# Performance work log

Hardware: AMD Instinct MI355X
Metric: run time of the kernel (lower is better)

Reference implementation:

```python
import jax, jax.numpy as jnp
import numpy as np

TINY = 1e-8
B, T, D = 128, 32, 400


def _offsets(T):
    offs, off = [], 0
    for lvl in range(T):
        offs.append(off)
        off += T - lvl
    return offs


def _inside_indices(T):
    # For level l, span start i (L = T - l spans), split k in [0, l):
    #   left child  = cell(offs[k] + i)             (span (i, level k))
    #   right child = cell(offs[l-k-1] + i + k + 1) (span (i+k+1, level l-k-1))
    offs = _offsets(T)
    out = {}
    for level in range(1, T):
        L = T - level
        lidx = np.empty((L, level), np.int32)
        ridx = np.empty((L, level), np.int32)
        for i in range(L):
            for k in range(level):
                lidx[i, k] = offs[k] + i
                ridx[i, k] = offs[level - k - 1] + i + k + 1
        out[level] = (jnp.asarray(lidx.reshape(-1)), jnp.asarray(ridx.reshape(-1)))
    return offs, out


def unit_norm(x):
    n = jnp.sqrt(jnp.sum(x * x, axis=-1, keepdims=True))
    return x / jnp.maximum(n, TINY)


def setup_inputs() -> dict:
    key = jax.random.key(0)
    ks = jax.random.split(key, 12)
    sc = 1.0 / np.sqrt(D).astype(np.float32)
    return {
        'x': jax.random.normal(ks[0], (B, T, D), jnp.float32),
        'w_leaf_h': jax.random.normal(ks[1], (D, D), jnp.float32) * sc,
        'b_leaf_h': jax.random.normal(ks[2], (D,), jnp.float32) * sc,
        'w_leaf_c': jax.random.normal(ks[3], (D, D), jnp.float32) * sc,
        'b_leaf_c': jax.random.normal(ks[4], (D,), jnp.float32) * sc,
        'u_lh': jax.random.normal(ks[5], (D, D), jnp.float32) * sc,
        'u_rh': jax.random.normal(ks[6], (D, D), jnp.float32) * sc,
        'b_h': jax.random.normal(ks[7], (D,), jnp.float32) * sc,
        'u_lc': jax.random.normal(ks[8], (D, D), jnp.float32) * sc,
        'u_rc': jax.random.normal(ks[9], (D, D), jnp.float32) * sc,
        'b_c': jax.random.normal(ks[10], (D,), jnp.float32) * sc,
        'w_score': jax.random.normal(ks[11], (D, D), jnp.float32) * sc,
    }


def reference(x, w_leaf_h, b_leaf_h, w_leaf_c, b_leaf_c,
              u_lh, u_rh, b_h, u_lc, u_rc, b_c, w_score):
    Bb, Tt, Dd = x.shape
    offs, idx = _inside_indices(Tt)
    ncells = Tt * (Tt + 1) // 2
    # leaf_transform + unit normalize
    h0 = unit_norm(jnp.tanh(x @ w_leaf_h + b_leaf_h))
    c0 = unit_norm(jnp.tanh(x @ w_leaf_c + b_leaf_c))
    ch = jnp.zeros((Bb, ncells, Dd), x.dtype).at[:, :Tt].set(h0)
    cc = jnp.zeros((Bb, ncells, Dd), x.dtype).at[:, :Tt].set(c0)
    cs = jnp.zeros((Bb, ncells, 1), x.dtype)
    for level in range(1, Tt):  # fixed structural loop over tree levels
        L, N = Tt - level, level
        lidx, ridx = idx[level]
        lh, rh = ch[:, lidx], ch[:, ridx]  # gather: [B, L*N, D]
        lc, rc = cc[:, lidx], cc[:, ridx]
        ls, rs = cs[:, lidx], cs[:, ridx]  # [B, L*N, 1]
        # compose
        h = jnp.tanh(lh @ u_lh + rh @ u_rh + b_h)
        c = jnp.tanh(lc @ u_lc + rc @ u_rc + b_c)
        # bilinear score + child scores, softmax over splits N
        s = jnp.einsum('bnd,de,bne->bn', lh, w_score, rh)[..., None] + ls + rs
        s = s.reshape(Bb, L, N, 1)
        p = jax.nn.softmax(s, axis=2)
        h_agg = unit_norm(jnp.sum(h.reshape(Bb, L, N, Dd) * p, axis=2))
        c_agg = unit_norm(jnp.sum(c.reshape(Bb, L, N, Dd) * p, axis=2))
        s_agg = jnp.sum(s * p, axis=2)
        off = offs[level]
        ch = ch.at[:, off:off + L].set(h_agg)
        cc = cc.at[:, off:off + L].set(c_agg)
        cs = cs.at[:, off:off + L].set(s_agg)
    return ch
```

## Files before the change

### kernel.cpp

```cpp
#include <hip/hip_runtime.h>
#include <hip/hip_bf16.h>
#include <stdint.h>


#define BB 128
#define TT 32
#define DD 400
#define NCELLS 528
#define NW 2000
#define KP 416

typedef __hip_bfloat16 bf16_t;
typedef __attribute__((ext_vector_type(8))) short s8v;
typedef __attribute__((ext_vector_type(4))) float f32x4;

__device__ __forceinline__ int offs_of(int v) { return v * TT - (v * (v - 1)) / 2; }

__device__ __forceinline__ float asf(uint32_t bits) {
    union { uint32_t i; float f; } v; v.i = bits; return v.f;
}
__device__ __forceinline__ uint16_t f2bf(float f) {
    union { float f; uint32_t i; } v; v.f = f;
    uint32_t x = v.i;
    return (uint16_t)((x + 0x7fffu + ((x >> 16) & 1u)) >> 16);
}

__device__ __forceinline__ float tanh_fast(float x) {
    float e = __builtin_amdgcn_exp2f(x * 2.8853900817779268f);
    return 1.f - 2.f * __builtin_amdgcn_rcpf(e + 1.f);
}

__device__ __forceinline__ void block_reduce2(float& a, float& b, float* sred) {
#pragma unroll
    for (int o = 32; o > 0; o >>= 1) { a += __shfl_down(a, o); b += __shfl_down(b, o); }
    int lane = threadIdx.x & 63, w = threadIdx.x >> 6;
    if (lane == 0) { sred[w] = a; sred[4 + w] = b; }
    __syncthreads();
    a = sred[0] + sred[1] + sred[2] + sred[3];
    b = sred[4] + sred[5] + sred[6] + sred[7];
    __syncthreads();
}

__global__ void pack_k(const float* __restrict__ u_lh, const float* __restrict__ u_rh,
                       const float* __restrict__ w_score, const float* __restrict__ u_lc,
                       const float* __restrict__ u_rc, const float* __restrict__ w_leaf_h,
                       const float* __restrict__ w_leaf_c, const float* __restrict__ x,
                       uint16_t* __restrict__ WT, uint16_t* __restrict__ WLT,
                       uint16_t* __restrict__ XB) {
    int idx = blockIdx.x * blockDim.x + threadIdx.x;
    const int nWT = NW * KP, nWLT = 800 * KP, nXB = 4096 * KP;
    if (idx < nWT) {
        int n = idx / KP, k = idx - n * KP;
        float v = 0.f;
        if (k < DD) {
            const float* src = (n < 400) ? u_lh : (n < 800) ? u_rh : (n < 1200) ? w_score
                               : (n < 1600) ? u_lc : u_rc;
            v = src[k * DD + (n % 400)];
        }
        WT[idx] = f2bf(v);
    } else if (idx < nWT + nWLT) {
        int q = idx - nWT; int n = q / KP, k = q - n * KP;
        float v = 0.f;
        if (k < DD) v = (n < 400) ? w_leaf_h[k * DD + n] : w_leaf_c[k * DD + (n - 400)];
        WLT[q] = f2bf(v);
    } else if (idx < nWT + nWLT + nXB) {
        int q = idx - nWT - nWLT; int r = q / KP, k = q - r * KP;
        XB[q] = f2bf(k < DD ? x[(size_t)r * DD + k] : 0.f);
    }
}

__global__ __launch_bounds__(256)
void tgemm_k(const uint16_t* __restrict__ HB, const uint16_t* __restrict__ CB,
             const uint16_t* __restrict__ WT,
             uint16_t* __restrict__ LP, uint16_t* __restrict__ RP, uint16_t* __restrict__ G,
             float* __restrict__ PREout, int mode, int Lcur, int cellbase) {
    __shared__ short As[256][40];
    __shared__ short Ws[80][40];
    const int t = threadIdx.x, lane = t & 63, w = t >> 6;
    const int n0 = blockIdx.x * 80;
    const int tile_m = blockIdx.y * 256;
    const bool cside = (mode == 0) && (n0 >= 1200);
    const int Mtot = (mode == 1) ? 4096 : 128 * Lcur;

    const int arow_l = t >> 2, asub = t & 3;
    const uint16_t* aptr[4];
#pragma unroll
    for (int p = 0; p < 4; p++) {
        int gr = tile_m + arow_l + 64 * p;
        if (gr >= Mtot) gr = 0;
        const uint16_t* base;
        if (mode == 1) {
            base = HB + (size_t)gr * KP;
        } else {
            int rb = gr / Lcur, ri = gr - rb * Lcur;
            base = cside ? CB + (size_t)(rb * 32 + ri) * DD
                         : HB + (size_t)(rb * NCELLS + cellbase + ri) * DD;
        }
        aptr[p] = base + asub * 8;
    }
    const uint16_t* wptr0 = WT + (size_t)(n0 + (t >> 2)) * KP + (t & 3) * 8;
    const uint16_t* wptr1 = WT + (size_t)(n0 + 64 + (t >> 2)) * KP + (t & 3) * 8;

    const int frow = lane & 15, kcol = (lane >> 4) * 8;
    f32x4 acc[4][5];
#pragma unroll
    for (int mi = 0; mi < 4; mi++)
#pragma unroll
        for (int ni = 0; ni < 5; ni++) acc[mi][ni] = (f32x4)(0.f);

    for (int k0 = 0; k0 < KP; k0 += 32) {
        s8v av[4];
#pragma unroll
        for (int p = 0; p < 4; p++) av[p] = *(const s8v*)(aptr[p] + k0);
        s8v wv0 = *(const s8v*)(wptr0 + k0);
        s8v wv1;
        if (t < 64) wv1 = *(const s8v*)(wptr1 + k0);
        __syncthreads();
#pragma unroll
        for (int p = 0; p < 4; p++) *(s8v*)&As[arow_l + 64 * p][asub * 8] = av[p];
        *(s8v*)&Ws[t >> 2][(t & 3) * 8] = wv0;
        if (t < 64) *(s8v*)&Ws[64 + (t >> 2)][(t & 3) * 8] = wv1;
        __syncthreads();
        s8v a[4];
#pragma unroll
        for (int mi = 0; mi < 4; mi++)
            a[mi] = *(const s8v*)&As[64 * w + 16 * mi + frow][kcol];
#pragma unroll
        for (int ni = 0; ni < 5; ni++) {
            s8v bv = *(const s8v*)&Ws[16 * ni + frow][kcol];
#pragma unroll
            for (int mi = 0; mi < 4; mi++)
                acc[mi][ni] = __builtin_amdgcn_mfma_f32_16x16x32_bf16(a[mi], bv, acc[mi][ni], 0, 0, 0);
        }
    }

    const int seg = n0 / 400, ncb = n0 % 400;
    uint16_t* tb = (seg == 2) ? G : (seg == 0 || seg == 3) ? LP : RP;
    const int slot = (seg >= 3) ? 1 : 0;
#pragma unroll
    for (int mi = 0; mi < 4; mi++) {
        int rbase = tile_m + 64 * w + 16 * mi + 4 * (lane >> 4);
#pragma unroll
        for (int i = 0; i < 4; i++) {
            int gr = rbase + i;
            if (gr >= Mtot) continue;
            if (mode == 1) {
                float* o = PREout + (size_t)gr * 800 + n0 + frow;
#pragma unroll
                for (int ni = 0; ni < 5; ni++) o[16 * ni] = acc[mi][ni][i];
            } else {
                int rb = gr / Lcur, ri = gr - rb * Lcur;
                size_t row = (size_t)(rb * NCELLS + cellbase + ri);
                if (seg == 2) {
                    uint16_t* o = tb + row * 400 + ncb + frow;
#pragma unroll
                    for (int ni = 0; ni < 5; ni++) o[16 * ni] = f2bf(acc[mi][ni][i]);
                } else {
                    uint16_t* o = tb + row * 800 + 2 * (ncb + frow) + slot;
#pragma unroll
                    for (int ni = 0; ni < 5; ni++) o[32 * ni] = f2bf(acc[mi][ni][i]);
                }
            }
        }
    }
}

__global__ __launch_bounds__(256)
void leaf_norm_k(const float* __restrict__ PRE, const float* __restrict__ blh,
                 const float* __restrict__ blc, float* __restrict__ Hchart,
                 uint16_t* __restrict__ HB, uint16_t* __restrict__ CB,
                 float* __restrict__ cs) {
    const int r = blockIdx.x;
    const int b = r >> 5, tt = r & 31;
    const int t = threadIdx.x;
    const int d = t * 2;
    float th0 = 0, th1 = 0, tc0 = 0, tc1 = 0;
    if (d < DD) {
        const float* p = PRE + (size_t)r * 800;
        th0 = tanh_fast(p[d] + blh[d]);
        th1 = tanh_fast(p[d + 1] + blh[d + 1]);
        tc0 = tanh_fast(p[400 + d] + blc[d]);
        tc1 = tanh_fast(p[400 + d + 1] + blc[d + 1]);
    }
    __shared__ float sred[8];
    float nh = th0 * th0 + th1 * th1, nc = tc0 * tc0 + tc1 * tc1;
    block_reduce2(nh, nc, sred);
    float rh = 1.f / fmaxf(sqrtf(nh), 1e-8f);
    float rc = 1.f / fmaxf(sqrtf(nc), 1e-8f);
    if (d < DD) {
        size_t ho = (size_t)(b * NCELLS + tt) * DD + d;
        float h0 = th0 * rh, h1 = th1 * rh, c0 = tc0 * rc, c1 = tc1 * rc;
        Hchart[ho] = h0; Hchart[ho + 1] = h1;
        *(uint32_t*)(HB + ho) = (uint32_t)f2bf(h0) | ((uint32_t)f2bf(h1) << 16);
        *(uint32_t*)(CB + (size_t)(b * 32 + tt) * DD + d) =
            (uint32_t)f2bf(c0) | ((uint32_t)f2bf(c1) << 16);
    }
    if (t == 0) cs[b * NCELLS + tt] = 0.f;
}

__global__ __launch_bounds__(256)
void level_k(float* __restrict__ Hchart, uint16_t* __restrict__ HB,
             uint16_t* __restrict__ CB, float* __restrict__ cs,
             const uint16_t* __restrict__ LP, const uint16_t* __restrict__ RP,
             const uint16_t* __restrict__ G,
             const float* __restrict__ b_h, const float* __restrict__ b_c, int level) {
    const int L = TT - level, N = level;
    const int blk = blockIdx.x;
    const int b = blk / L, i = blk - b * L;
    const int cell = offs_of(level) + i;
    const int t = threadIdx.x, lane = t & 63, w = t >> 6;
    __shared__ float sh_s[32], sh_p[32];
    __shared__ float sred[8];

    for (int k = w; k < N; k += 4) {
        int lcell = offs_of(k) + i;
        int rcell = offs_of(level - k - 1) + i + k + 1;
        const uint32_t* g = (const uint32_t*)(G + (size_t)(b * NCELLS + lcell) * DD);
        const uint32_t* hr = (const uint32_t*)(HB + (size_t)(b * NCELLS + rcell) * DD);
        float s = 0.f;
        for (int d2 = lane; d2 < 200; d2 += 64) {
            uint32_t gv = g[d2], hv = hr[d2];
            s += asf(gv << 16) * asf(hv << 16)
               + asf(gv & 0xffff0000u) * asf(hv & 0xffff0000u);
        }
#pragma unroll
        for (int o = 32; o > 0; o >>= 1) s += __shfl_down(s, o);
        if (lane == 0) sh_s[k] = s + cs[b * NCELLS + lcell] + cs[b * NCELLS + rcell];
    }
    __syncthreads();

    if (t == 0) {
        float m = -1e30f;
        for (int k = 0; k < N; k++) m = fmaxf(m, sh_s[k]);
        float sum = 0.f;
        for (int k = 0; k < N; k++) {
            float e = __builtin_amdgcn_exp2f((sh_s[k] - m) * 1.4426950408889634f);
            sh_p[k] = e; sum += e;
        }
        float inv = 1.f / sum, sagg = 0.f;
        for (int k = 0; k < N; k++) { sh_p[k] *= inv; sagg += sh_p[k] * sh_s[k]; }
        cs[b * NCELLS + cell] = sagg;
    }
    __syncthreads();

    float ha0 = 0, ha1 = 0, ca0 = 0, ca1 = 0;
    const int d = t * 2;
    if (d < DD) {
        const float bh0 = b_h[d], bh1 = b_h[d + 1], bc0 = b_c[d], bc1 = b_c[d + 1];
        const uint16_t* lpb = LP + (size_t)(b * NCELLS) * 800 + 2 * d;
        const uint16_t* rpb = RP + (size_t)(b * NCELLS) * 800 + 2 * d;
        for (int k = 0; k < N; k++) {
            float p = sh_p[k];
            int lcell = offs_of(k) + i;
            int rcell = offs_of(level - k - 1) + i + k + 1;
            uint2 lv = *(const uint2*)(lpb + (size_t)lcell * 800);
            uint2 rv = *(const uint2*)(rpb + (size_t)rcell * 800);
            ha0 += p * tanh_fast(asf(lv.x << 16) + asf(rv.x << 16) + bh0);
            ca0 += p * tanh_fast(asf(lv.x & 0xffff0000u) + asf(rv.x & 0xffff0000u) + bc0);
            ha1 += p * tanh_fast(asf(lv.y << 16) + asf(rv.y << 16) + bh1);
            ca1 += p * tanh_fast(asf(lv.y & 0xffff0000u) + asf(rv.y & 0xffff0000u) + bc1);
        }
    }
    float nh = ha0 * ha0 + ha1 * ha1, nc = ca0 * ca0 + ca1 * ca1;
    block_reduce2(nh, nc, sred);
    float rh = 1.f / fmaxf(sqrtf(nh), 1e-8f);
    float rc = 1.f / fmaxf(sqrtf(nc), 1e-8f);
    if (d < DD) {
        float h0 = ha0 * rh, h1 = ha1 * rh, c0 = ca0 * rc, c1 = ca1 * rc;
        size_t ho = (size_t)(b * NCELLS + cell) * DD + d;
        Hchart[ho] = h0; Hchart[ho + 1] = h1;
        *(uint32_t*)(HB + ho) = (uint32_t)f2bf(h0) | ((uint32_t)f2bf(h1) << 16);
        *(uint32_t*)(CB + (size_t)(b * 32 + i) * DD + d) =
            (uint32_t)f2bf(c0) | ((uint32_t)f2bf(c1) << 16);
    }
}

extern "C" void kernel_launch(void* const* d_in, const int* in_sizes, int n_in,
                              void* d_out, int out_size, void* d_ws, size_t ws_size,
                              hipStream_t stream) {
    const float* x        = (const float*)d_in[0];
    const float* w_leaf_h = (const float*)d_in[1];
    const float* b_leaf_h = (const float*)d_in[2];
    const float* w_leaf_c = (const float*)d_in[3];
    const float* b_leaf_c = (const float*)d_in[4];
    const float* u_lh     = (const float*)d_in[5];
    const float* u_rh     = (const float*)d_in[6];
    const float* b_h      = (const float*)d_in[7];
    const float* u_lc     = (const float*)d_in[8];
    const float* u_rc     = (const float*)d_in[9];
    const float* b_c      = (const float*)d_in[10];
    const float* w_score  = (const float*)d_in[11];
    float* Hchart = (float*)d_out;

    const size_t PL = (size_t)BB * NCELLS * DD;
    char* p = (char*)d_ws;
    uint16_t* LP = (uint16_t*)p; p += 2 * PL * sizeof(uint16_t);
    uint16_t* RP = (uint16_t*)p; p += 2 * PL * sizeof(uint16_t);
    uint16_t* G  = (uint16_t*)p; p += PL * sizeof(uint16_t);
    uint16_t* HB = (uint16_t*)p; p += PL * sizeof(uint16_t) + 64;
    uint16_t* CB = (uint16_t*)p; p += (size_t)BB * 32 * DD * sizeof(uint16_t) + 64;
    float* CS    = (float*)p;    p += (size_t)BB * NCELLS * sizeof(float);
    uint16_t* WT = (uint16_t*)p; p += (size_t)NW * KP * sizeof(uint16_t);
    float* PRE    = (float*)LP;
    uint16_t* WLT = RP;
    uint16_t* XB  = RP + (size_t)800 * KP;

    {
        int total = NW * KP + 800 * KP + 4096 * KP;
        pack_k<<<(total + 255) / 256, 256, 0, stream>>>(u_lh, u_rh, w_score, u_lc, u_rc,
                                                        w_leaf_h, w_leaf_c, x, WT, WLT, XB);
    }
    tgemm_k<<<dim3(10, 16), 256, 0, stream>>>(XB, nullptr, WLT, nullptr, nullptr, nullptr,
                                              PRE, 1, 32, 0);
    leaf_norm_k<<<BB * TT, 256, 0, stream>>>(PRE, b_leaf_h, b_leaf_c, Hchart, HB, CB, CS);
    tgemm_k<<<dim3(25, 16), 256, 0, stream>>>(HB, CB, WT, LP, RP, G, nullptr, 0, 32, 0);

    int off = TT;
    for (int level = 1; level < TT; ++level) {
        int L = TT - level;
        level_k<<<BB * L, 256, 0, stream>>>(Hchart, HB, CB, CS, LP, RP, G, b_h, b_c, level);
        if (level < TT - 1) {
            int mby = (128 * L + 255) / 256;
            tgemm_k<<<dim3(25, mby), 256, 0, stream>>>(HB, CB, WT, LP, RP, G, nullptr, 0, L, off);
        }
        off += L;
    }
}
```

Baseline: 1.648 ms.

## Fuse per-level kernels into one persistent cooperative kernel with grid sync

Replaces the roughly 61 per-level kernel launches (level_k plus tgemm_k for each tree level) with a single cooperative persistent kernel. Blocks loop over level cells and GEMM tiles and separate phases with grid.sync(). The GEMM tiles shrink from 256 to 128 rows so the small upper levels have more tiles to spread across the grid. This removes launch overhead and tail gaps between many small kernels, at the cost of grid-wide barriers, capped occupancy (launch bounds 256,2), and a fallback path if the cooperative launch fails.

```diff
diff --git a/kernel.cpp b/kernel.cpp
--- a/kernel.cpp
+++ b/kernel.cpp
@@ -1,6 +1,9 @@
 #include <hip/hip_runtime.h>
+#include <hip/hip_cooperative_groups.h>
 #include <hip/hip_bf16.h>
 #include <stdint.h>
+
+namespace cg = cooperative_groups;
 
 
 #define BB 128
@@ -10,7 +13,6 @@
 #define NW 2000
 #define KP 416
 
-typedef __hip_bfloat16 bf16_t;
 typedef __attribute__((ext_vector_type(8))) short s8v;
 typedef __attribute__((ext_vector_type(4))) float f32x4;
 
@@ -24,7 +26,6 @@
     uint32_t x = v.i;
     return (uint16_t)((x + 0x7fffu + ((x >> 16) & 1u)) >> 16);
 }
-
 __device__ __forceinline__ float tanh_fast(float x) {
     float e = __builtin_amdgcn_exp2f(x * 2.8853900817779268f);
     return 1.f - 2.f * __builtin_amdgcn_rcpf(e + 1.f);
@@ -69,16 +70,14 @@
     }
 }
 
-__global__ __launch_bounds__(256)
-void tgemm_k(const uint16_t* __restrict__ HB, const uint16_t* __restrict__ CB,
-             const uint16_t* __restrict__ WT,
-             uint16_t* __restrict__ LP, uint16_t* __restrict__ RP, uint16_t* __restrict__ G,
-             float* __restrict__ PREout, int mode, int Lcur, int cellbase) {
-    __shared__ short As[256][40];
-    __shared__ short Ws[80][40];
+__device__ __forceinline__
+void tgemm_tile(const uint16_t* __restrict__ HB, const uint16_t* __restrict__ CB,
+                const uint16_t* __restrict__ WT,
+                uint16_t* __restrict__ LP, uint16_t* __restrict__ RP,
+                uint16_t* __restrict__ G, float* __restrict__ PREout,
+                int mode, int Lcur, int cellbase, int n0, int tile_m,
+                short (*As)[40], short (*Ws)[40]) {
     const int t = threadIdx.x, lane = t & 63, w = t >> 6;
-    const int n0 = blockIdx.x * 80;
-    const int tile_m = blockIdx.y * 256;
     const bool cside = (mode == 0) && (n0 >= 1200);
     const int Mtot = (mode == 1) ? 4096 : 128 * Lcur;
 
@@ -160,6 +159,93 @@
 #pragma unroll
                     for (int ni = 0; ni < 5; ni++) o[32 * ni] = f2bf(acc[mi][ni][i]);
                 }
+            }
+        }
+    }
+}
+
+__global__ __launch_bounds__(256)
+void tgemm_k(const uint16_t* __restrict__ HB, const uint16_t* __restrict__ CB,
+             const uint16_t* __restrict__ WT,
+             uint16_t* __restrict__ LP, uint16_t* __restrict__ RP, uint16_t* __restrict__ G,
+             float* __restrict__ PREout, int mode, int Lcur, int cellbase) {
+    __shared__ short As[256][40];
+    __shared__ short Ws[80][40];
+    tgemm_tile(HB, CB, WT, LP, RP, G, PREout, mode, Lcur, cellbase,
+               blockIdx.x * 80, blockIdx.y * 256, As, Ws);
+}
+
+__device__ __forceinline__
+void tgemm_tile128(const uint16_t* __restrict__ HB, const uint16_t* __restrict__ CB,
+                   const uint16_t* __restrict__ WT,
+                   uint16_t* __restrict__ LP, uint16_t* __restrict__ RP,
+                   uint16_t* __restrict__ G,
+                   int Lcur, int cellbase, int n0, int tile_m,
+                   short (*As)[40], short (*Ws)[40]) {
+    const int t = threadIdx.x, lane = t & 63, w = t >> 6;
+    const bool cside = (n0 >= 1200);
+
+    const int arow_l = t >> 2, asub = t & 3;
+    const uint16_t* aptr[2];
+#pragma unroll
+    for (int p = 0; p < 2; p++) {
+        int gr = tile_m + arow_l + 64 * p;
+        int rb = gr / Lcur, ri = gr - rb * Lcur;
+        const uint16_t* base = cside ? CB + (size_t)(rb * 32 + ri) * DD
+                                     : HB + (size_t)(rb * NCELLS + cellbase + ri) * DD;
+        aptr[p] = base + asub * 8;
+    }
+    const uint16_t* wptr0 = WT + (size_t)(n0 + (t >> 2)) * KP + (t & 3) * 8;
+    const uint16_t* wptr1 = WT + (size_t)(n0 + 64 + (t >> 2)) * KP + (t & 3) * 8;
+
+    const int frow = lane & 15, kcol = (lane >> 4) * 8;
+    f32x4 acc[2][5];
+#pragma unroll
+    for (int mi = 0; mi < 2; mi++)
+#pragma unroll
+        for (int ni = 0; ni < 5; ni++) acc[mi][ni] = (f32x4)(0.f);
+
+    for (int k0 = 0; k0 < KP; k0 += 32) {
+        s8v av0 = *(const s8v*)(aptr[0] + k0);
+        s8v av1 = *(const s8v*)(aptr[1] + k0);
+        s8v wv0 = *(const s8v*)(wptr0 + k0);
+        s8v wv1;
+        if (t < 64) wv1 = *(const s8v*)(wptr1 + k0);
+        __syncthreads();
+        *(s8v*)&As[arow_l][asub * 8] = av0;
+        *(s8v*)&As[arow_l + 64][asub * 8] = av1;
+        *(s8v*)&Ws[t >> 2][(t & 3) * 8] = wv0;
+        if (t < 64) *(s8v*)&Ws[64 + (t >> 2)][(t & 3) * 8] = wv1;
+        __syncthreads();
+        s8v a0 = *(const s8v*)&As[32 * w + frow][kcol];
+        s8v a1 = *(const s8v*)&As[32 * w + 16 + frow][kcol];
+#pragma unroll
+        for (int ni = 0; ni < 5; ni++) {
+            s8v bv = *(const s8v*)&Ws[16 * ni + frow][kcol];
+            acc[0][ni] = __builtin_amdgcn_mfma_f32_16x16x32_bf16(a0, bv, acc[0][ni], 0, 0, 0);
+            acc[1][ni] = __builtin_amdgcn_mfma_f32_16x16x32_bf16(a1, bv, acc[1][ni], 0, 0, 0);
+        }
+    }
+
+    const int seg = n0 / 400, ncb = n0 % 400;
+    uint16_t* tb = (seg == 2) ? G : (seg == 0 || seg == 3) ? LP : RP;
+    const int slot = (seg >= 3) ? 1 : 0;
+#pragma unroll
+    for (int mi = 0; mi < 2; mi++) {
+        int rbase = tile_m + 32 * w + 16 * mi + 4 * (lane >> 4);
+#pragma unroll
+        for (int i = 0; i < 4; i++) {
+            int gr = rbase + i;
+            int rb = gr / Lcur, ri = gr - rb * Lcur;
+            size_t row = (size_t)(rb * NCELLS + cellbase + ri);
+            if (seg == 2) {
+                uint16_t* o = tb + row * 400 + ncb + frow;
+#pragma unroll
+                for (int ni = 0; ni < 5; ni++) o[16 * ni] = f2bf(acc[mi][ni][i]);
+            } else {
+                uint16_t* o = tb + row * 800 + 2 * (ncb + frow) + slot;
+#pragma unroll
+                for (int ni = 0; ni < 5; ni++) o[32 * ni] = f2bf(acc[mi][ni][i]);
             }
         }
     }
@@ -198,19 +284,17 @@
     if (t == 0) cs[b * NCELLS + tt] = 0.f;
 }
 
-__global__ __launch_bounds__(256)
-void level_k(float* __restrict__ Hchart, uint16_t* __restrict__ HB,
-             uint16_t* __restrict__ CB, float* __restrict__ cs,
-             const uint16_t* __restrict__ LP, const uint16_t* __restrict__ RP,
-             const uint16_t* __restrict__ G,
-             const float* __restrict__ b_h, const float* __restrict__ b_c, int level) {
-    const int L = TT - level, N = level;
-    const int blk = blockIdx.x;
-    const int b = blk / L, i = blk - b * L;
+__device__ void level_cell(float* __restrict__ Hchart, uint16_t* __restrict__ HB,
+                           uint16_t* __restrict__ CB, float* __restrict__ cs,
+                           const uint16_t* __restrict__ LP, const uint16_t* __restrict__ RP,
+                           const uint16_t* __restrict__ G,
+                           const float* __restrict__ b_h, const float* __restrict__ b_c,
+                           int level, int b, int i,
+                           float* sh_s, float* sh_p, float* sred) {
+    const int N = level;
     const int cell = offs_of(level) + i;
     const int t = threadIdx.x, lane = t & 63, w = t >> 6;
-    __shared__ float sh_s[32], sh_p[32];
-    __shared__ float sred[8];
+    __syncthreads();
 
     for (int k = w; k < N; k += 4) {
         int lcell = offs_of(k) + i;
@@ -275,6 +359,52 @@
     }
 }
 
+__global__ __launch_bounds__(256)
+void level_k(float* __restrict__ Hchart, uint16_t* __restrict__ HB,
+             uint16_t* __restrict__ CB, float* __restrict__ cs,
+             const uint16_t* __restrict__ LP, const uint16_t* __restrict__ RP,
+             const uint16_t* __restrict__ G,
+             const float* __restrict__ b_h, const float* __restrict__ b_c, int level) {
+    __shared__ float sh_s[32], sh_p[32], sred[8];
+    const int L = TT - level;
+    int b = blockIdx.x / L, i = blockIdx.x - b * L;
+    level_cell(Hchart, HB, CB, cs, LP, RP, G, b_h, b_c, level, b, i, sh_s, sh_p, sred);
+}
+
+struct CoopArgs {
+    float* Hchart; uint16_t* HB; uint16_t* CB; float* CS;
+    uint16_t* LP; uint16_t* RP; uint16_t* G; const uint16_t* WT;
+    const float* b_h; const float* b_c;
+};
+
+__global__ __launch_bounds__(256, 2)
+void diora_levels_k(CoopArgs A) {
+    __shared__ short As[128][40];
+    __shared__ short Ws[80][40];
+    __shared__ float sh_s[32], sh_p[32], sred[8];
+    cg::grid_group grid = cg::this_grid();
+
+    int off = TT;
+    for (int level = 1; level < TT; ++level) {
+        const int L = TT - level;
+        for (int ci = blockIdx.x; ci < BB * L; ci += gridDim.x) {
+            int b = ci / L, i = ci - b * L;
+            level_cell(A.Hchart, A.HB, A.CB, A.CS, A.LP, A.RP, A.G,
+                       A.b_h, A.b_c, level, b, i, sh_s, sh_p, sred);
+        }
+        grid.sync();
+        if (level < TT - 1) {
+            const int ntiles = 25 * L;
+            for (int tile = blockIdx.x; tile < ntiles; tile += gridDim.x) {
+                tgemm_tile128(A.HB, A.CB, A.WT, A.LP, A.RP, A.G,
+                              L, off, (tile % 25) * 80, (tile / 25) * 128, As, Ws);
+            }
+            grid.sync();
+        }
+        off += L;
+    }
+}
+
 extern "C" void kernel_launch(void* const* d_in, const int* in_sizes, int n_in,
                               void* d_out, int out_size, void* d_ws, size_t ws_size,
                               hipStream_t stream) {
@@ -315,14 +445,29 @@
     leaf_norm_k<<<BB * TT, 256, 0, stream>>>(PRE, b_leaf_h, b_leaf_c, Hchart, HB, CB, CS);
     tgemm_k<<<dim3(25, 16), 256, 0, stream>>>(HB, CB, WT, LP, RP, G, nullptr, 0, 32, 0);
 
-    int off = TT;
-    for (int level = 1; level < TT; ++level) {
-        int L = TT - level;
-        level_k<<<BB * L, 256, 0, stream>>>(Hchart, HB, CB, CS, LP, RP, G, b_h, b_c, level);
-        if (level < TT - 1) {
-            int mby = (128 * L + 255) / 256;
-            tgemm_k<<<dim3(25, mby), 256, 0, stream>>>(HB, CB, WT, LP, RP, G, nullptr, 0, L, off);
-        }
-        off += L;
-    }
-}
+    int occ = 0;
+    hipError_t qerr = hipOccupancyMaxActiveBlocksPerMultiprocessor(
+        &occ, (const void*)diora_levels_k, 256, 0);
+    if (qerr != hipSuccess || occ < 1) occ = 1;
+    int nblk = occ * 256;
+    if (nblk > 1024) nblk = 1024;
+
+    CoopArgs ca{Hchart, HB, CB, CS, LP, RP, G, WT, b_h, b_c};
+    void* kargs[] = {&ca};
+    hipError_t lerr = hipLaunchCooperativeKernel((void*)diora_levels_k, dim3(nblk),
+                                                 dim3(256), kargs, 0, stream);
+    if (lerr != hipSuccess) {
+        int off = TT;
+        for (int level = 1; level < TT; ++level) {
+            int L = TT - level;
+            level_k<<<BB * L, 256, 0, stream>>>(Hchart, HB, CB, CS, LP, RP, G,
+                                                b_h, b_c, level);
+            if (level < TT - 1) {
+                int mby = (128 * L + 255) / 256;
+                tgemm_k<<<dim3(25, mby), 256, 0, stream>>>(HB, CB, WT, LP, RP, G,
+                                                           nullptr, 0, L, off);
+            }
+            off += L;
+        }
+    }
+}
```

Result: slower. 5.798 ms (+251.7%).

## Split projection GEMM into paired h/c kernel with packed 32-bit stores

Applied to the files above, without the earlier changes.

Replaces the mode-switched GEMM for the per-level child projections with a dedicated kernel that computes the h-side and c-side projections for the same output column chunk in one block. The two results are packed into one 32-bit store instead of two strided 16-bit stores. M tiles shrink to 128 rows, so each level launches about twice as many blocks, which suits small levels with few rows. The leaf GEMM is simplified to a single-mode kernel. The cost is more registers and shared memory per block and an uneven load between the blocks that compute both h and c and the score-only blocks.

```diff
diff --git a/kernel.cpp b/kernel.cpp
--- a/kernel.cpp
+++ b/kernel.cpp
@@ -10,7 +10,6 @@
 #define NW 2000
 #define KP 416
 
-typedef __hip_bfloat16 bf16_t;
 typedef __attribute__((ext_vector_type(8))) short s8v;
 typedef __attribute__((ext_vector_type(4))) float f32x4;
 
@@ -24,7 +23,6 @@
     uint32_t x = v.i;
     return (uint16_t)((x + 0x7fffu + ((x >> 16) & 1u)) >> 16);
 }
-
 __device__ __forceinline__ float tanh_fast(float x) {
     float e = __builtin_amdgcn_exp2f(x * 2.8853900817779268f);
     return 1.f - 2.f * __builtin_amdgcn_rcpf(e + 1.f);
@@ -70,36 +68,23 @@
 }
 
 __global__ __launch_bounds__(256)
-void tgemm_k(const uint16_t* __restrict__ HB, const uint16_t* __restrict__ CB,
-             const uint16_t* __restrict__ WT,
-             uint16_t* __restrict__ LP, uint16_t* __restrict__ RP, uint16_t* __restrict__ G,
-             float* __restrict__ PREout, int mode, int Lcur, int cellbase) {
+void tgemm_k(const uint16_t* __restrict__ XB, const uint16_t* __restrict__ WLT,
+             float* __restrict__ PREout) {
     __shared__ short As[256][40];
     __shared__ short Ws[80][40];
     const int t = threadIdx.x, lane = t & 63, w = t >> 6;
     const int n0 = blockIdx.x * 80;
     const int tile_m = blockIdx.y * 256;
-    const bool cside = (mode == 0) && (n0 >= 1200);
-    const int Mtot = (mode == 1) ? 4096 : 128 * Lcur;
 
     const int arow_l = t >> 2, asub = t & 3;
     const uint16_t* aptr[4];
 #pragma unroll
     for (int p = 0; p < 4; p++) {
         int gr = tile_m + arow_l + 64 * p;
-        if (gr >= Mtot) gr = 0;
-        const uint16_t* base;
-        if (mode == 1) {
-            base = HB + (size_t)gr * KP;
-        } else {
-            int rb = gr / Lcur, ri = gr - rb * Lcur;
-            base = cside ? CB + (size_t)(rb * 32 + ri) * DD
-                         : HB + (size_t)(rb * NCELLS + cellbase + ri) * DD;
-        }
-        aptr[p] = base + asub * 8;
-    }
-    const uint16_t* wptr0 = WT + (size_t)(n0 + (t >> 2)) * KP + (t & 3) * 8;
-    const uint16_t* wptr1 = WT + (size_t)(n0 + 64 + (t >> 2)) * KP + (t & 3) * 8;
+        aptr[p] = XB + (size_t)gr * KP + asub * 8;
+    }
+    const uint16_t* wptr0 = WLT + (size_t)(n0 + (t >> 2)) * KP + (t & 3) * 8;
+    const uint16_t* wptr1 = WLT + (size_t)(n0 + 64 + (t >> 2)) * KP + (t & 3) * 8;
 
     const int frow = lane & 15, kcol = (lane >> 4) * 8;
     f32x4 acc[4][5];
@@ -133,33 +118,132 @@
                 acc[mi][ni] = __builtin_amdgcn_mfma_f32_16x16x32_bf16(a[mi], bv, acc[mi][ni], 0, 0, 0);
         }
     }
-
-    const int seg = n0 / 400, ncb = n0 % 400;
-    uint16_t* tb = (seg == 2) ? G : (seg == 0 || seg == 3) ? LP : RP;
-    const int slot = (seg >= 3) ? 1 : 0;
 #pragma unroll
     for (int mi = 0; mi < 4; mi++) {
         int rbase = tile_m + 64 * w + 16 * mi + 4 * (lane >> 4);
 #pragma unroll
         for (int i = 0; i < 4; i++) {
             int gr = rbase + i;
-            if (gr >= Mtot) continue;
-            if (mode == 1) {
-                float* o = PREout + (size_t)gr * 800 + n0 + frow;
-#pragma unroll
-                for (int ni = 0; ni < 5; ni++) o[16 * ni] = acc[mi][ni][i];
-            } else {
+            float* o = PREout + (size_t)gr * 800 + n0 + frow;
+#pragma unroll
+            for (int ni = 0; ni < 5; ni++) o[16 * ni] = acc[mi][ni][i];
+        }
+    }
+}
+
+__global__ __launch_bounds__(256)
+void tpgemm_k(const uint16_t* __restrict__ HB, const uint16_t* __restrict__ CB,
+              const uint16_t* __restrict__ WT,
+              uint16_t* __restrict__ LP, uint16_t* __restrict__ RP,
+              uint16_t* __restrict__ G, int Lcur, int cellbase) {
+    __shared__ short AsH[128][40];
+    __shared__ short AsC[128][40];
+    __shared__ short WsH[80][40];
+    __shared__ short WsC[80][40];
+    const int t = threadIdx.x, lane = t & 63, w = t >> 6;
+    const int nch = blockIdx.x % 5, kind = blockIdx.x / 5;
+    const int n0 = nch * 80;
+    const int tile_m = blockIdx.y * 128;
+    const bool doC = (kind != 2);
+
+    const int wh0 = (kind == 0) ? n0 : (kind == 1) ? 400 + n0 : 800 + n0;
+    const int wc0 = (kind == 0) ? 1200 + n0 : 1600 + n0;
+
+    const int arow_l = t >> 2, asub = t & 3;
+    const uint16_t *aptrH[2], *aptrC[2];
+#pragma unroll
+    for (int p = 0; p < 2; p++) {
+        int gr = tile_m + arow_l + 64 * p;
+        int rb = gr / Lcur, ri = gr - rb * Lcur;
+        aptrH[p] = HB + (size_t)(rb * NCELLS + cellbase + ri) * DD + asub * 8;
+        aptrC[p] = CB + (size_t)(rb * 32 + ri) * DD + asub * 8;
+    }
+    const uint16_t* wptrH0 = WT + (size_t)(wh0 + (t >> 2)) * KP + (t & 3) * 8;
+    const uint16_t* wptrH1 = WT + (size_t)(wh0 + 64 + (t >> 2)) * KP + (t & 3) * 8;
+    const uint16_t* wptrC0 = WT + (size_t)(wc0 + (t >> 2)) * KP + (t & 3) * 8;
+    const uint16_t* wptrC1 = WT + (size_t)(wc0 + 64 + (t >> 2)) * KP + (t & 3) * 8;
+
+    const int frow = lane & 15, kcol = (lane >> 4) * 8;
+    f32x4 accH[2][5], accC[2][5];
+#pragma unroll
+    for (int mi = 0; mi < 2; mi++)
+#pragma unroll
+        for (int ni = 0; ni < 5; ni++) { accH[mi][ni] = (f32x4)(0.f); accC[mi][ni] = (f32x4)(0.f); }
+
+    for (int k0 = 0; k0 < KP; k0 += 32) {
+        s8v avH0 = *(const s8v*)(aptrH[0] + k0);
+        s8v avH1 = *(const s8v*)(aptrH[1] + k0);
+        s8v wvH0 = *(const s8v*)(wptrH0 + k0);
+        s8v wvH1;
+        if (t < 64) wvH1 = *(const s8v*)(wptrH1 + k0);
+        s8v avC0, avC1, wvC0, wvC1;
+        if (doC) {
+            avC0 = *(const s8v*)(aptrC[0] + k0);
+            avC1 = *(const s8v*)(aptrC[1] + k0);
+            wvC0 = *(const s8v*)(wptrC0 + k0);
+            if (t < 64) wvC1 = *(const s8v*)(wptrC1 + k0);
+        }
+        __syncthreads();
+        *(s8v*)&AsH[arow_l][asub * 8] = avH0;
+        *(s8v*)&AsH[arow_l + 64][asub * 8] = avH1;
+        *(s8v*)&WsH[t >> 2][(t & 3) * 8] = wvH0;
+        if (t < 64) *(s8v*)&WsH[64 + (t >> 2)][(t & 3) * 8] = wvH1;
+        if (doC) {
+            *(s8v*)&AsC[arow_l][asub * 8] = avC0;
+            *(s8v*)&AsC[arow_l + 64][asub * 8] = avC1;
+            *(s8v*)&WsC[t >> 2][(t & 3) * 8] = wvC0;
+            if (t < 64) *(s8v*)&WsC[64 + (t >> 2)][(t & 3) * 8] = wvC1;
+        }
+        __syncthreads();
+        s8v aH0 = *(const s8v*)&AsH[32 * w + frow][kcol];
+        s8v aH1 = *(const s8v*)&AsH[32 * w + 16 + frow][kcol];
+        s8v aC0, aC1;
+        if (doC) {
+            aC0 = *(const s8v*)&AsC[32 * w + frow][kcol];
+            aC1 = *(const s8v*)&AsC[32 * w + 16 + frow][kcol];
+        }
+#pragma unroll
+        for (int ni = 0; ni < 5; ni++) {
+            s8v bvH = *(const s8v*)&WsH[16 * ni + frow][kcol];
+            accH[0][ni] = __builtin_amdgcn_mfma_f32_16x16x32_bf16(aH0, bvH, accH[0][ni], 0, 0, 0);
+            accH[1][ni] = __builtin_amdgcn_mfma_f32_16x16x32_bf16(aH1, bvH, accH[1][ni], 0, 0, 0);
+            if (doC) {
+                s8v bvC = *(const s8v*)&WsC[16 * ni + frow][kcol];
+                accC[0][ni] = __builtin_amdgcn_mfma_f32_16x16x32_bf16(aC0, bvC, accC[0][ni], 0, 0, 0);
+                accC[1][ni] = __builtin_amdgcn_mfma_f32_16x16x32_bf16(aC1, bvC, accC[1][ni], 0, 0, 0);
+            }
+        }
+    }
+
+    if (kind == 2) {
+#pragma unroll
+        for (int mi = 0; mi < 2; mi++) {
+            int rbase = tile_m + 32 * w + 16 * mi + 4 * (lane >> 4);
+#pragma unroll
+            for (int i = 0; i < 4; i++) {
+                int gr = rbase + i;
                 int rb = gr / Lcur, ri = gr - rb * Lcur;
                 size_t row = (size_t)(rb * NCELLS + cellbase + ri);
-                if (seg == 2) {
-                    uint16_t* o = tb + row * 400 + ncb + frow;
-#pragma unroll
-                    for (int ni = 0; ni < 5; ni++) o[16 * ni] = f2bf(acc[mi][ni][i]);
-                } else {
-                    uint16_t* o = tb + row * 800 + 2 * (ncb + frow) + slot;
-#pragma unroll
-                    for (int ni = 0; ni < 5; ni++) o[32 * ni] = f2bf(acc[mi][ni][i]);
-                }
+                uint16_t* o = G + row * 400 + n0 + frow;
+#pragma unroll
+                for (int ni = 0; ni < 5; ni++) o[16 * ni] = f2bf(accH[mi][ni][i]);
+            }
+        }
+    } else {
+        uint16_t* tb = (kind == 0) ? LP : RP;
+#pragma unroll
+        for (int mi = 0; mi < 2; mi++) {
+            int rbase = tile_m + 32 * w + 16 * mi + 4 * (lane >> 4);
+#pragma unroll
+            for (int i = 0; i < 4; i++) {
+                int gr = rbase + i;
+                int rb = gr / Lcur, ri = gr - rb * Lcur;
+                size_t row = (size_t)(rb * NCELLS + cellbase + ri);
+                uint32_t* o = (uint32_t*)(tb + row * 800) + n0 + frow;
+#pragma unroll
+                for (int ni = 0; ni < 5; ni++)
+                    o[16 * ni] = (uint32_t)f2bf(accH[mi][ni][i])
+                               | ((uint32_t)f2bf(accC[mi][ni][i]) << 16);
             }
         }
     }
@@ -310,18 +394,16 @@
         pack_k<<<(total + 255) / 256, 256, 0, stream>>>(u_lh, u_rh, w_score, u_lc, u_rc,
                                                         w_leaf_h, w_leaf_c, x, WT, WLT, XB);
     }
-    tgemm_k<<<dim3(10, 16), 256, 0, stream>>>(XB, nullptr, WLT, nullptr, nullptr, nullptr,
-                                              PRE, 1, 32, 0);
+    tgemm_k<<<dim3(10, 16), 256, 0, stream>>>(XB, WLT, PRE);
     leaf_norm_k<<<BB * TT, 256, 0, stream>>>(PRE, b_leaf_h, b_leaf_c, Hchart, HB, CB, CS);
-    tgemm_k<<<dim3(25, 16), 256, 0, stream>>>(HB, CB, WT, LP, RP, G, nullptr, 0, 32, 0);
+    tpgemm_k<<<dim3(15, 32), 256, 0, stream>>>(HB, CB, WT, LP, RP, G, 32, 0);
 
     int off = TT;
     for (int level = 1; level < TT; ++level) {
         int L = TT - level;
         level_k<<<BB * L, 256, 0, stream>>>(Hchart, HB, CB, CS, LP, RP, G, b_h, b_c, level);
         if (level < TT - 1) {
-            int mby = (128 * L + 255) / 256;
-            tgemm_k<<<dim3(25, mby), 256, 0, stream>>>(HB, CB, WT, LP, RP, G, nullptr, 0, L, off);
+            tpgemm_k<<<dim3(15, L), 256, 0, stream>>>(HB, CB, WT, LP, RP, G, L, off);
         }
         off += L;
     }
```

Measured after the change: 1.664 ms. About the same (+1.0%).
